# Kernel tuning notes

Measured on AMD Instinct MI355X. Metric: run time of the kernel, lower is better.

The kernel has to match this reference:

```python
import jax, jax.numpy as jnp
import numpy as np

D = 128  # time-encoder dimension == attention embed_dim


def harmonic_encode(ts, basis_freq):
    # ts: (N,) -> (N, D); phases are zero in the original module
    m = ts[:, None] * basis_freq[None, :]
    return jnp.sqrt(1.0 / D) * jnp.concatenate([jnp.cos(m), jnp.sin(m)], axis=1)


def mha_1head(q, k, mask, Wq, bq, Wk, bk, Wv, bv, Wo, bo):
    # Single-head nn.MultiheadAttention. q: (T, D) queries (torch batch dim),
    # k: (S, D) shared keys/values (original repeats these T times; same math),
    # mask: (T, S) True = masked out (key_padding_mask semantics).
    qp = q @ Wq.T + bq
    kp = k @ Wk.T + bk
    vp = k @ Wv.T + bv
    scores = jnp.einsum('td,sd->ts', qp, kp) / jnp.sqrt(jnp.asarray(D, q.dtype))
    scores = jnp.where(mask, -jnp.inf, scores)
    attn = jax.nn.softmax(scores, axis=-1)  # (T, S)
    return (attn @ vp) @ Wo.T + bo


def setup_inputs() -> dict:
    key = jax.random.key(0)
    ks = jax.random.split(key, 24)
    T, L, V = 4096, 8192, 1000
    s = 1.0 / np.sqrt(D)
    inp = {
        't': jax.random.uniform(ks[0], (T,), jnp.float32),
        'e_nodes_ts': jax.random.uniform(ks[1], (L,), jnp.float32),
        'e_nodes_exp': jax.random.randint(ks[2], (L,), 0, V),
        'e_node_target': jax.random.randint(ks[3], (1,), 0, V),
        'basis_freq': jnp.asarray(1.0 / 5.0 ** np.linspace(1, 9, D // 2), jnp.float32),
        'phi': jnp.ones((1,), jnp.float32),
        'W_lin': jax.random.normal(ks[4], (1, 2 * D), jnp.float32) * 0.05,
        'b_lin': jnp.zeros((1,), jnp.float32),
    }
    kidx = 5
    for suf in ('_s', '_n'):
        for nm in ('Wq', 'Wk', 'Wv', 'Wo'):
            inp[nm + suf] = jax.random.normal(ks[kidx], (D, D), jnp.float32) * s
            kidx += 1
        for nm in ('bq', 'bk', 'bv', 'bo'):
            inp[nm + suf] = jnp.zeros((D,), jnp.float32)
    return inp


def reference(t, e_nodes_ts, e_nodes_exp, e_node_target, basis_freq, phi, W_lin, b_lin,
              Wq_s, Wk_s, Wv_s, Wo_s, bq_s, bk_s, bv_s, bo_s,
              Wq_n, Wk_n, Wv_n, Wo_n, bq_n, bk_n, bv_n, bo_n):
    # prepend sentinels exactly as the torch forward does
    ts_all = jnp.concatenate([jnp.zeros((2,), e_nodes_ts.dtype), e_nodes_ts])      # (S,)
    exp_all = jnp.concatenate([jnp.full((1,), -1, e_nodes_exp.dtype), e_node_target, e_nodes_exp])  # (S,)

    phi_t = harmonic_encode(t, basis_freq)        # (T, D)
    phi_ts = harmonic_encode(ts_all, basis_freq)  # (S, D)

    pad = ts_all[None, :] > t[:, None]            # (T, S) future events masked
    self_mask = pad | (exp_all != e_node_target[0])[None, :]
    neig_mask = pad | (exp_all == e_node_target[0])[None, :]

    out_s = mha_1head(phi_t, phi_ts, self_mask, Wq_s, bq_s, Wk_s, bk_s, Wv_s, bv_s, Wo_s, bo_s)
    out_n = mha_1head(phi_t, phi_ts, neig_mask, Wq_n, bq_n, Wk_n, bk_n, Wv_n, bv_n, Wo_n, bo_n)
    atten_output = jnp.concatenate([out_s, out_n], axis=1)  # (T, 2D)

    lam = atten_output @ W_lin.T + b_lin          # (T, 1)
    x = lam * phi
    x = jnp.where(x > 20.0, 20.0, x)              # clamp as in soft_plus()
    lambdav = (1.0 / phi) * jnp.log1p(jnp.exp(x))
    return lambdav, atten_output
```

## Files before the change

### kernel.cpp

```cpp
#include <hip/hip_runtime.h>

#define T_Q 4096
#define S_TOT 8194
#define S_ALLOC 8256
#define SELF_CAP 128
#define NSEG 11
#define NSLOT 12
#define NCH64 129
#define SCALE 0.08838834764831843f
#define NEG_BIG -1.0e30f
#define TS_INF 3.0e38f

typedef __attribute__((ext_vector_type(8))) short short8;
typedef __attribute__((ext_vector_type(4))) float f32x4;
typedef __attribute__((ext_vector_type(4))) unsigned short ush4;
typedef unsigned short ush;
typedef unsigned int uint32;
typedef unsigned long long u64;

static __device__ __forceinline__ ush f2bf(float f) {
    unsigned int u = __float_as_uint(f);
    u += 0x7FFFu + ((u >> 16) & 1u);
    return (ush)(u >> 16);
}

__global__ __launch_bounds__(256) void prep_kernel(
    const float* __restrict__ t, const float* __restrict__ ets,
    const int* __restrict__ exps, const int* __restrict__ tgtp,
    const float* __restrict__ bf,
    const float* __restrict__ Wo_s, const float* __restrict__ Wv_s, const float* __restrict__ bv_s,
    const float* __restrict__ Wo_n, const float* __restrict__ Wv_n, const float* __restrict__ bv_n,
    const float* __restrict__ Wq_s, const float* __restrict__ Wq_n,
    const float* __restrict__ Wk_s, const float* __restrict__ Wk_n,
    ush* __restrict__ phi_t, ush* __restrict__ phi_ts,
    float* __restrict__ ts_pad, float* __restrict__ ts1, int* __restrict__ perm1,
    u64* __restrict__ maskbits, ush* __restrict__ Wb, float* __restrict__ bvo)
{
    __shared__ float red[256];
    __shared__ int swcnt[4];
    __shared__ int stot;
    int bid = blockIdx.x, tid = threadIdx.x;

    if (bid < 3088) {
        int R = bid * 4 + (tid >> 6);
        int j = tid & 63;
        float x; ush* dst;
        if (R < T_Q) { x = t[R]; dst = phi_t + (size_t)R * 128; }
        else {
            int s = R - T_Q;
            x = (s < 2) ? 0.0f : ((s < S_TOT) ? ets[s - 2] : 0.0f);
            dst = phi_ts + (size_t)s * 128;
        }
        float m = x * bf[j];
        dst[j]      = f2bf(cosf(m) * SCALE);
        dst[64 + j] = f2bf(sinf(m) * SCALE);
    } else if (bid == 3088) {
        int tgt = tgtp[0];
        for (int i = tid; i < S_ALLOC; i += 256)
            ts_pad[i] = (i < 2) ? 0.f : ((i < S_TOT) ? ets[i - 2] : TS_INF);
        int w4 = tid >> 6, lane = tid & 63;
        int cbeg = w4 * 33, cend = (w4 == 3) ? NCH64 : (cbeg + 33);
        u64 ltm = ((u64)1 << lane) - 1ull;
        int cnt = 0;
        for (int ch = cbeg; ch < cend; ++ch) {
            int s = ch * 64 + lane;
            bool m = (s < S_TOT) && ((s == 1) || (s >= 2 && exps[s - 2] == tgt));
            u64 b = __ballot(m);
            if (lane == 0) maskbits[ch] = b;
            cnt += __popcll(b);
        }
        if (lane == 0) swcnt[w4] = cnt;
        __syncthreads();
        if (tid == 0) {
            int a = 0;
            #pragma unroll
            for (int i = 0; i < 4; ++i) { int tc = swcnt[i]; swcnt[i] = a; a += tc; }
            stot = a;
        }
        __syncthreads();
        int off2 = swcnt[w4];
        for (int ch = cbeg; ch < cend; ++ch) {
            int s = ch * 64 + lane;
            bool m = (s < S_TOT) && ((s == 1) || (s >= 2 && exps[s - 2] == tgt));
            u64 b = __ballot(m);
            if (m) {
                int p = off2 + __popcll(b & ltm);
                if (p < SELF_CAP) { perm1[p] = s; ts1[p] = (s >= 2) ? ets[s - 2] : 0.f; }
            }
            off2 += __popcll(b);
        }
        __syncthreads();
        int st = stot > SELF_CAP ? SELF_CAP : stot;
        for (int i = st + tid; i < SELF_CAP; i += 256) { perm1[i] = 0; ts1[i] = TS_INF; }
    } else if (bid < 3217) {
        int row = bid - 3089;
        int h = tid >> 7, col = tid & 127;
        const float* Wo = h ? Wo_n : Wo_s;
        const float* Wv = h ? Wv_n : Wv_s;
        const float* bv = h ? bv_n : bv_s;
        float acc = 0.f;
        for (int jj = 0; jj < 128; ++jj) acc += Wo[row * 128 + jj] * Wv[jj * 128 + col];
        Wb[(size_t)(4 + h) * 16384 + row * 128 + col] = f2bf(acc);
        red[tid] = Wo[row * 128 + col] * bv[col];
        __syncthreads();
        for (int off = 64; off > 0; off >>= 1) {
            if ((tid & 127) < off) red[tid] += red[tid + off];
            __syncthreads();
        }
        if ((tid & 127) == 0) bvo[h * 128 + row] = red[tid];
    } else {
        int idx = (bid - 3217) * 256 + tid;
        int which = idx >> 14, e = idx & 16383;
        const float* src;
        switch (which) {
            case 0: src = Wq_s; break; case 1: src = Wq_n; break;
            case 2: src = Wk_s; break; default: src = Wk_n; break;
        }
        Wb[idx] = f2bf(src[e]);
    }
}

__global__ __launch_bounds__(256) void proj_kernel(
    const ush* __restrict__ phi_t, const ush* __restrict__ phi_ts, const ush* __restrict__ Wb,
    const float* __restrict__ bq_s, const float* __restrict__ bq_n,
    const float* __restrict__ bk_s, const float* __restrict__ bk_n,
    const float* __restrict__ bvo, const int* __restrict__ perm1,
    ush* __restrict__ qp, ush* __restrict__ kpc, ush* __restrict__ vpoT)
{
    int y = blockIdx.y;
    const float* b; int M; const int* perm = nullptr; int ldv = 0;
    const ush* in = phi_ts;
    ush* out = nullptr; ush* outT = nullptr;
    switch (y) {
        case 0: b = bq_s;      M = T_Q; in = phi_t; out = qp; break;
        case 1: b = bq_n;      M = T_Q; in = phi_t; out = qp + (size_t)T_Q * 128; break;
        case 2: b = bk_s;      M = SELF_CAP; perm = perm1; out = kpc; break;
        case 3: b = bk_n;      M = S_ALLOC;  out = kpc + (size_t)SELF_CAP * 128; break;
        case 4: b = bvo;       M = SELF_CAP; perm = perm1; outT = vpoT; ldv = SELF_CAP; break;
        default:b = bvo + 128; M = S_ALLOC;  outT = vpoT + (size_t)SELF_CAP * 128; ldv = S_ALLOC; break;
    }
    int mbase = blockIdx.x * 64 + (int)(threadIdx.x >> 6) * 16;
    if (mbase >= M) return;
    int lane = threadIdx.x & 63, u = lane >> 4, c = lane & 15;
    const ush* arow = perm ? (in + (size_t)perm[mbase + c] * 128)
                           : (in + (size_t)(mbase + c) * 128);
    short8 af[4];
    #pragma unroll
    for (int ks = 0; ks < 4; ++ks) af[ks] = *(const short8*)(arow + ks * 32 + u * 8);
    const ush* W = Wb + (size_t)y * 16384;
    #pragma unroll
    for (int nt = 0; nt < 8; ++nt) {
        int ncol = nt * 16 + c;
        float bval = b[ncol];
        f32x4 acc = {bval, bval, bval, bval};
        #pragma unroll
        for (int ks = 0; ks < 4; ++ks) {
            short8 bf8 = *(const short8*)(W + ncol * 128 + ks * 32 + u * 8);
            acc = __builtin_amdgcn_mfma_f32_16x16x32_bf16(af[ks], bf8, acc, 0, 0, 0);
        }
        if (outT) {
            ush4 pk;
            #pragma unroll
            for (int r = 0; r < 4; ++r) pk[r] = f2bf(acc[r]);
            *(ush4*)(outT + (size_t)ncol * ldv + mbase + u * 4) = pk;
        } else {
            #pragma unroll
            for (int r = 0; r < 4; ++r)
                out[(size_t)(mbase + u * 4 + r) * 128 + ncol] = f2bf(acc[r]);
        }
    }
}

__global__ __launch_bounds__(256, 2) void attn_kernel(
    const ush* __restrict__ qp, const ush* __restrict__ kpc, const ush* __restrict__ vpoT,
    const float* __restrict__ ts_pad, const float* __restrict__ ts1,
    const u64* __restrict__ maskbits, const float* __restrict__ tq,
    float* __restrict__ Opart, float* __restrict__ mpart, float* __restrict__ lpart)
{
    int bid = blockIdx.x;
    int head, qb, slot, t0, t1;
    if (bid < 32 * NSEG) {
        head = 1; int seg = bid >> 5; qb = bid & 31; slot = seg;
        t0 = seg * NCH64 / NSEG; t1 = (seg + 1) * NCH64 / NSEG;
    } else {
        head = 0; qb = bid - 32 * NSEG; slot = NSEG; t0 = 0; t1 = SELF_CAP / 64;
    }
    const ush* kph = kpc  + (head ? (size_t)SELF_CAP * 128 : 0);
    const ush* vph = vpoT + (head ? (size_t)SELF_CAP * 128 : 0);
    const int ld = head ? S_ALLOC : SELF_CAP;
    const float* tsh = head ? ts_pad : ts1;
    const ush* qph = qp + (head ? (size_t)T_Q * 128 : 0);

    __shared__ __align__(16) ush K2[2][64 * 128];
    __shared__ __align__(16) ush V1[128 * 64];
    __shared__ float tsb[2][64];

    int tid = threadIdx.x, w = tid >> 6, lane = tid & 63;
    int u = lane >> 4, c = lane & 15;
    int qrow0 = qb * 128 + w * 32;
    int sbase = (lane & 48) + ((lane & 48) >> 2);

    short8 qf[2][4];
    #pragma unroll
    for (int qg = 0; qg < 2; ++qg) {
        const ush* qr = qph + (size_t)(qrow0 + qg * 16 + c) * 128;
        #pragma unroll
        for (int ks = 0; ks < 4; ++ks) qf[qg][ks] = *(const short8*)(qr + ks * 32 + u * 8);
    }
    float t_c[2] = { tq[qrow0 + c], tq[qrow0 + 16 + c] };

    f32x4 Ov[2][8];
    #pragma unroll
    for (int qg = 0; qg < 2; ++qg)
        #pragma unroll
        for (int dt = 0; dt < 8; ++dt) Ov[qg][dt] = (f32x4){0.f, 0.f, 0.f, 0.f};
    float mrow[2] = {NEG_BIG, NEG_BIG}, lrow[2] = {0.f, 0.f};

    short8 kreg[4], vreg[4]; float tsreg = 0.f;
    int kr = tid >> 2, kq = tid & 3;
    int vd = tid >> 1, vh = tid & 1;

    auto LOADT = [&](int t) {
        int kb = t * 64;
        const ush* src = kph + (size_t)(kb + kr) * 128 + kq * 32;
        #pragma unroll
        for (int i = 0; i < 4; ++i) kreg[i] = *(const short8*)(src + i * 8);
        const ush* vsrc = vph + (size_t)vd * ld + kb + vh * 32;
        #pragma unroll
        for (int i = 0; i < 4; ++i) vreg[i] = *(const short8*)(vsrc + i * 8);
        if (tid < 64) tsreg = tsh[kb + tid];
    };
    auto WRITE_K = [&](int b) {
        #pragma unroll
        for (int i = 0; i < 4; ++i)
            *(short8*)&K2[b][kr * 128 + (((kq * 4 + i) ^ (kr & 7)) << 3)] = kreg[i];
        if (tid < 64) tsb[b][tid] = tsreg;
    };
    auto WRITE_V = [&]() {
        #pragma unroll
        for (int i = 0; i < 4; ++i)
            *(short8*)&V1[vd * 64 + (((vh * 4 + i) ^ (vd & 7)) << 3)] = vreg[i];
    };

    LOADT(t0); WRITE_K(0); WRITE_V();
    __syncthreads();

    for (int t = t0; t < t1; ++t) {
        int cur = (t - t0) & 1;
        bool pre = (t + 1 < t1);
        u64 mk = head ? maskbits[t] : 0ull;
        if (pre) LOADT(t + 1);

        float sc[2][4][4];
        #pragma unroll
        for (int ct = 0; ct < 4; ++ct) {
            short8 kf[4];
            int row = ct * 16 + c;
            #pragma unroll
            for (int ks = 0; ks < 4; ++ks)
                kf[ks] = *(const short8*)&K2[cur][row * 128 + (((ks * 4 + u) ^ (row & 7)) << 3)];
            f32x4 acc0 = {0.f, 0.f, 0.f, 0.f}, acc1 = {0.f, 0.f, 0.f, 0.f};
            #pragma unroll
            for (int ks = 0; ks < 4; ++ks) {
                acc0 = __builtin_amdgcn_mfma_f32_16x16x32_bf16(kf[ks], qf[0][ks], acc0, 0, 0, 0);
                acc1 = __builtin_amdgcn_mfma_f32_16x16x32_bf16(kf[ks], qf[1][ks], acc1, 0, 0, 0);
            }
            f32x4 ts4 = *(const f32x4*)&tsb[cur][ct * 16 + u * 4];
            uint32 mh = (uint32)(mk >> (ct * 16 + u * 4));
            #pragma unroll
            for (int r = 0; r < 4; ++r) {
                bool em = (mh >> r) & 1u;
                sc[0][ct][r] = (em || ts4[r] > t_c[0]) ? NEG_BIG : acc0[r] * SCALE;
                sc[1][ct][r] = (em || ts4[r] > t_c[1]) ? NEG_BIG : acc1[r] * SCALE;
            }
        }
        if (pre) WRITE_K(cur ^ 1);

        short8 pfq[2][2];
        #pragma unroll
        for (int qg = 0; qg < 2; ++qg) {
            float mt = sc[qg][0][0];
            #pragma unroll
            for (int ct = 0; ct < 4; ++ct)
                #pragma unroll
                for (int r = 0; r < 4; ++r) mt = fmaxf(mt, sc[qg][ct][r]);
            mt = fmaxf(mt, __shfl_xor(mt, 16));
            mt = fmaxf(mt, __shfl_xor(mt, 32));
            if (__any(mt > mrow[qg])) {
                float mnew = fmaxf(mrow[qg], mt);
                float sf = __expf(mrow[qg] - mnew);
                mrow[qg] = mnew;
                lrow[qg] *= sf;
                float sfr[4];
                #pragma unroll
                for (int r = 0; r < 4; ++r) sfr[r] = __shfl(sf, sbase + r);
                #pragma unroll
                for (int dt = 0; dt < 8; ++dt) {
                    Ov[qg][dt][0] *= sfr[0]; Ov[qg][dt][1] *= sfr[1];
                    Ov[qg][dt][2] *= sfr[2]; Ov[qg][dt][3] *= sfr[3];
                }
            }
            float p[4][4], s16 = 0.f;
            #pragma unroll
            for (int ct = 0; ct < 4; ++ct)
                #pragma unroll
                for (int r = 0; r < 4; ++r) { p[ct][r] = __expf(sc[qg][ct][r] - mrow[qg]); s16 += p[ct][r]; }
            s16 += __shfl_xor(s16, 16);
            s16 += __shfl_xor(s16, 32);
            lrow[qg] += s16;

            uint32 q0[4], q1[4];
            #pragma unroll
            for (int ct = 0; ct < 4; ++ct) {
                asm("v_cvt_pk_bf16_f32 %0, %1, %2" : "=v"(q0[ct]) : "v"(p[ct][0]), "v"(p[ct][1]));
                asm("v_cvt_pk_bf16_f32 %0, %1, %2" : "=v"(q1[ct]) : "v"(p[ct][2]), "v"(p[ct][3]));
            }
            #pragma unroll
            for (int ksl = 0; ksl < 2; ++ksl) {
                uint32 a0 = q0[2 * ksl], b0 = q0[2 * ksl + 1];
                uint32 a1 = q1[2 * ksl], b1 = q1[2 * ksl + 1];
                asm("v_permlane32_swap_b32 %0, %1" : "+v"(a0), "+v"(b0));
                asm("v_permlane16_swap_b32 %0, %1" : "+v"(a0), "+v"(b0));
                asm("v_permlane32_swap_b32 %0, %1" : "+v"(a1), "+v"(b1));
                asm("v_permlane16_swap_b32 %0, %1" : "+v"(a1), "+v"(b1));
                union { uint32 w4[4]; short8 s8; } pk_;
                pk_.w4[0] = a0; pk_.w4[1] = a1; pk_.w4[2] = b0; pk_.w4[3] = b1;
                pfq[qg][ksl] = pk_.s8;
            }
        }

        #pragma unroll
        for (int ksl = 0; ksl < 2; ++ksl)
            #pragma unroll
            for (int dt = 0; dt < 8; ++dt) {
                int d = dt * 16 + c;
                short8 vf = *(const short8*)&V1[d * 64 + (((ksl * 4 + u) ^ (d & 7)) << 3)];
                Ov[0][dt] = __builtin_amdgcn_mfma_f32_16x16x32_bf16(pfq[0][ksl], vf, Ov[0][dt], 0, 0, 0);
                Ov[1][dt] = __builtin_amdgcn_mfma_f32_16x16x32_bf16(pfq[1][ksl], vf, Ov[1][dt], 0, 0, 0);
            }

        __syncthreads();
        if (pre) WRITE_V();
        __syncthreads();
    }

    size_t rbase = (size_t)slot * T_Q + qrow0;
    #pragma unroll
    for (int qg = 0; qg < 2; ++qg)
        #pragma unroll
        for (int dt = 0; dt < 8; ++dt)
            #pragma unroll
            for (int r = 0; r < 4; ++r)
                Opart[(rbase + qg * 16 + u * 4 + r) * 128 + dt * 16 + c] = Ov[qg][dt][r];
    if (u == 0) {
        mpart[rbase + c] = mrow[0];      lpart[rbase + c] = lrow[0];
        mpart[rbase + 16 + c] = mrow[1]; lpart[rbase + 16 + c] = lrow[1];
    }
}

__global__ __launch_bounds__(256) void combine_kernel(
    const float* __restrict__ Opart, const float* __restrict__ mpart, const float* __restrict__ lpart,
    const float* __restrict__ bo_s, const float* __restrict__ bo_n,
    const float* __restrict__ Wl, const float* __restrict__ bl,
    const float* __restrict__ phi, float* __restrict__ outp)
{
    int row = blockIdx.x, tid = threadIdx.x;
    float outv;
    if (tid < 128) {
        size_t rb = (size_t)NSEG * T_Q + row;
        outv = Opart[rb * 128 + tid] / lpart[rb] + bo_s[tid];
    } else {
        int d = tid - 128;
        float M = NEG_BIG;
        #pragma unroll
        for (int z = 0; z < NSEG; ++z) M = fmaxf(M, mpart[(size_t)z * T_Q + row]);
        float L = 0.f, O = 0.f;
        #pragma unroll
        for (int z = 0; z < NSEG; ++z) {
            size_t rb = (size_t)z * T_Q + row;
            float wz = __expf(mpart[rb] - M);
            L += wz * lpart[rb];
            O += wz * Opart[rb * 128 + d];
        }
        outv = O / L + bo_n[d];
    }
    outp[T_Q + (size_t)row * 256 + tid] = outv;

    float dot = outv * Wl[tid];
    #pragma unroll
    for (int off = 1; off < 64; off <<= 1) dot += __shfl_xor(dot, off);
    __shared__ float wsum[4];
    if ((tid & 63) == 0) wsum[tid >> 6] = dot;
    __syncthreads();
    if (tid == 0) {
        float s = wsum[0] + wsum[1] + wsum[2] + wsum[3];
        float ph = phi[0];
        float x = (s + bl[0]) * ph;
        x = fminf(x, 20.0f);
        outp[row] = log1pf(__expf(x)) / ph;
    }
}

extern "C" void kernel_launch(void* const* d_in, const int* in_sizes, int n_in,
                              void* d_out, int out_size, void* d_ws, size_t ws_size,
                              hipStream_t stream) {
    (void)in_sizes; (void)n_in; (void)out_size; (void)ws_size;
    const float* t    = (const float*)d_in[0];
    const float* ets  = (const float*)d_in[1];
    const int*   exps = (const int*)d_in[2];
    const int*   tgt  = (const int*)d_in[3];
    const float* bfq  = (const float*)d_in[4];
    const float* phi  = (const float*)d_in[5];
    const float* Wlin = (const float*)d_in[6];
    const float* blin = (const float*)d_in[7];
    const float* Wq_s = (const float*)d_in[8];
    const float* Wk_s = (const float*)d_in[9];
    const float* Wv_s = (const float*)d_in[10];
    const float* Wo_s = (const float*)d_in[11];
    const float* bq_s = (const float*)d_in[12];
    const float* bk_s = (const float*)d_in[13];
    const float* bv_s = (const float*)d_in[14];
    const float* bo_s = (const float*)d_in[15];
    const float* Wq_n = (const float*)d_in[16];
    const float* Wk_n = (const float*)d_in[17];
    const float* Wv_n = (const float*)d_in[18];
    const float* Wo_n = (const float*)d_in[19];
    const float* bq_n = (const float*)d_in[20];
    const float* bk_n = (const float*)d_in[21];
    const float* bv_n = (const float*)d_in[22];
    const float* bo_n = (const float*)d_in[23];

    char* ws = (char*)d_ws;
    size_t off = 0;
    auto alloc = [&](size_t bytes) { void* p = ws + off; off += (bytes + 255) & ~(size_t)255; return p; };
    ush* phi_t  = (ush*)alloc((size_t)T_Q * 128 * 2);
    ush* phi_ts = (ush*)alloc((size_t)S_ALLOC * 128 * 2);
    ush* qpb    = (ush*)alloc((size_t)2 * T_Q * 128 * 2);
    ush* kpc    = (ush*)alloc((size_t)(SELF_CAP + S_ALLOC) * 128 * 2);
    ush* vpoT   = (ush*)alloc((size_t)128 * (SELF_CAP + S_ALLOC) * 2);
    int*    perm1 = (int*)   alloc((size_t)SELF_CAP * 4);
    float*  ts1   = (float*) alloc((size_t)SELF_CAP * 4);
    float*  ts_pad= (float*) alloc((size_t)S_ALLOC * 4);
    u64*    maskb = (u64*)   alloc((size_t)NCH64 * 8);
    float*  bvo   = (float*) alloc((size_t)2 * 128 * 4);
    ush*    Wb    = (ush*)   alloc((size_t)6 * 16384 * 2);
    float*  Opart = (float*) alloc((size_t)NSLOT * T_Q * 128 * 4);
    float*  mpart = (float*) alloc((size_t)NSLOT * T_Q * 4);
    float*  lpart = (float*) alloc((size_t)NSLOT * T_Q * 4);

    float* outp = (float*)d_out;

    prep_kernel<<<dim3(3473), dim3(256), 0, stream>>>(
        t, ets, exps, tgt, bfq, Wo_s, Wv_s, bv_s, Wo_n, Wv_n, bv_n,
        Wq_s, Wq_n, Wk_s, Wk_n, phi_t, phi_ts, ts_pad, ts1, perm1, maskb, Wb, bvo);
    proj_kernel<<<dim3(129, 6), dim3(256), 0, stream>>>(
        phi_t, phi_ts, Wb, bq_s, bq_n, bk_s, bk_n, bvo, perm1, qpb, kpc, vpoT);
    attn_kernel<<<dim3(32 * NSEG + 32), dim3(256), 0, stream>>>(
        qpb, kpc, vpoT, ts_pad, ts1, maskb, t, Opart, mpart, lpart);
    combine_kernel<<<dim3(T_Q), dim3(256), 0, stream>>>(
        Opart, mpart, lpart, bo_s, bo_n, Wlin, blin, phi, outp);
}
```

Baseline: 106.6 us.

## Split neighbor attention into more segments, raise occupancy, store bf16 partials

Doubles the number of key segments for the neighbor head and remaps block indices with an interleaved order. Drops K double-buffering so the attention kernel uses less LDS and can run 3 blocks per SM. It now writes partial outputs in bf16, halving partial traffic in the combine step. Prep stages the expert ids in LDS as 16-bit values and unrolls the Wo·Wv product loop. The trade-offs are lost load/compute overlap on K, more partials to merge, and bf16 rounding of the unnormalized partial sums.

Result: slower. 170.2 us (+59.7%).

```diff
diff --git a/kernel.cpp b/kernel.cpp
--- a/kernel.cpp
+++ b/kernel.cpp
@@ -4,8 +4,8 @@
 #define S_TOT 8194
 #define S_ALLOC 8256
 #define SELF_CAP 128
-#define NSEG 11
-#define NSLOT 12
+#define NSEG 23
+#define NSLOT 24
 #define NCH64 129
 #define SCALE 0.08838834764831843f
 #define NEG_BIG -1.0e30f
@@ -22,6 +22,9 @@
     unsigned int u = __float_as_uint(f);
     u += 0x7FFFu + ((u >> 16) & 1u);
     return (ush)(u >> 16);
+}
+static __device__ __forceinline__ float bf2f(ush u) {
+    return __uint_as_float(((unsigned int)u) << 16);
 }
 
 __global__ __launch_bounds__(256) void prep_kernel(
@@ -36,9 +39,10 @@
     float* __restrict__ ts_pad, float* __restrict__ ts1, int* __restrict__ perm1,
     u64* __restrict__ maskbits, ush* __restrict__ Wb, float* __restrict__ bvo)
 {
-    __shared__ float red[256];
+    __shared__ __align__(16) ush es[8192];
     __shared__ int swcnt[4];
     __shared__ int stot;
+    float* red = (float*)es;
     int bid = blockIdx.x, tid = threadIdx.x;
 
     if (bid < 3088) {
@@ -56,15 +60,21 @@
         dst[64 + j] = f2bf(sinf(m) * SCALE);
     } else if (bid == 3088) {
         int tgt = tgtp[0];
+        for (int i = tid * 4; i < S_TOT - 2; i += 1024) {
+            int4 v = *(const int4*)(exps + i);
+            es[i] = (ush)v.x; es[i + 1] = (ush)v.y; es[i + 2] = (ush)v.z; es[i + 3] = (ush)v.w;
+        }
         for (int i = tid; i < S_ALLOC; i += 256)
             ts_pad[i] = (i < 2) ? 0.f : ((i < S_TOT) ? ets[i - 2] : TS_INF);
+        __syncthreads();
+        ush tgt16 = (ush)tgt;
         int w4 = tid >> 6, lane = tid & 63;
         int cbeg = w4 * 33, cend = (w4 == 3) ? NCH64 : (cbeg + 33);
         u64 ltm = ((u64)1 << lane) - 1ull;
         int cnt = 0;
         for (int ch = cbeg; ch < cend; ++ch) {
             int s = ch * 64 + lane;
-            bool m = (s < S_TOT) && ((s == 1) || (s >= 2 && exps[s - 2] == tgt));
+            bool m = (s < S_TOT) && ((s == 1) || (s >= 2 && es[s - 2] == tgt16));
             u64 b = __ballot(m);
             if (lane == 0) maskbits[ch] = b;
             cnt += __popcll(b);
@@ -81,7 +91,7 @@
         int off2 = swcnt[w4];
         for (int ch = cbeg; ch < cend; ++ch) {
             int s = ch * 64 + lane;
-            bool m = (s < S_TOT) && ((s == 1) || (s >= 2 && exps[s - 2] == tgt));
+            bool m = (s < S_TOT) && ((s == 1) || (s >= 2 && es[s - 2] == tgt16));
             u64 b = __ballot(m);
             if (m) {
                 int p = off2 + __popcll(b & ltm);
@@ -99,6 +109,7 @@
         const float* Wv = h ? Wv_n : Wv_s;
         const float* bv = h ? bv_n : bv_s;
         float acc = 0.f;
+        #pragma unroll 8
         for (int jj = 0; jj < 128; ++jj) acc += Wo[row * 128 + jj] * Wv[jj * 128 + col];
         Wb[(size_t)(4 + h) * 16384 + row * 128 + col] = f2bf(acc);
         red[tid] = Wo[row * 128 + col] * bv[col];
@@ -171,13 +182,13 @@
     }
 }
 
-__global__ __launch_bounds__(256, 2) void attn_kernel(
+__global__ __launch_bounds__(256, 3) void attn_kernel(
     const ush* __restrict__ qp, const ush* __restrict__ kpc, const ush* __restrict__ vpoT,
     const float* __restrict__ ts_pad, const float* __restrict__ ts1,
     const u64* __restrict__ maskbits, const float* __restrict__ tq,
-    float* __restrict__ Opart, float* __restrict__ mpart, float* __restrict__ lpart)
+    ush* __restrict__ Opart, float* __restrict__ mpart, float* __restrict__ lpart)
 {
-    int bid = blockIdx.x;
+    int bid = ((int)blockIdx.x & 7) * 96 + ((int)blockIdx.x >> 3);
     int head, qb, slot, t0, t1;
     if (bid < 32 * NSEG) {
         head = 1; int seg = bid >> 5; qb = bid & 31; slot = seg;
@@ -191,9 +202,9 @@
     const float* tsh = head ? ts_pad : ts1;
     const ush* qph = qp + (head ? (size_t)T_Q * 128 : 0);
 
-    __shared__ __align__(16) ush K2[2][64 * 128];
+    __shared__ __align__(16) ush K1[64 * 128];
     __shared__ __align__(16) ush V1[128 * 64];
-    __shared__ float tsb[2][64];
+    __shared__ float tsb[64];
 
     int tid = threadIdx.x, w = tid >> 6, lane = tid & 63;
     int u = lane >> 4, c = lane & 15;
@@ -230,23 +241,20 @@
         for (int i = 0; i < 4; ++i) vreg[i] = *(const short8*)(vsrc + i * 8);
         if (tid < 64) tsreg = tsh[kb + tid];
     };
-    auto WRITE_K = [&](int b) {
+    auto WRITE_KV = [&]() {
         #pragma unroll
         for (int i = 0; i < 4; ++i)
-            *(short8*)&K2[b][kr * 128 + (((kq * 4 + i) ^ (kr & 7)) << 3)] = kreg[i];
-        if (tid < 64) tsb[b][tid] = tsreg;
-    };
-    auto WRITE_V = [&]() {
+            *(short8*)&K1[kr * 128 + (((kq * 4 + i) ^ (kr & 7)) << 3)] = kreg[i];
         #pragma unroll
         for (int i = 0; i < 4; ++i)
             *(short8*)&V1[vd * 64 + (((vh * 4 + i) ^ (vd & 7)) << 3)] = vreg[i];
+        if (tid < 64) tsb[tid] = tsreg;
     };
 
-    LOADT(t0); WRITE_K(0); WRITE_V();
+    LOADT(t0); WRITE_KV();
     __syncthreads();
 
     for (int t = t0; t < t1; ++t) {
-        int cur = (t - t0) & 1;
         bool pre = (t + 1 < t1);
         u64 mk = head ? maskbits[t] : 0ull;
         if (pre) LOADT(t + 1);
@@ -258,14 +266,14 @@
             int row = ct * 16 + c;
             #pragma unroll
             for (int ks = 0; ks < 4; ++ks)
-                kf[ks] = *(const short8*)&K2[cur][row * 128 + (((ks * 4 + u) ^ (row & 7)) << 3)];
+                kf[ks] = *(const short8*)&K1[row * 128 + (((ks * 4 + u) ^ (row & 7)) << 3)];
             f32x4 acc0 = {0.f, 0.f, 0.f, 0.f}, acc1 = {0.f, 0.f, 0.f, 0.f};
             #pragma unroll
             for (int ks = 0; ks < 4; ++ks) {
                 acc0 = __builtin_amdgcn_mfma_f32_16x16x32_bf16(kf[ks], qf[0][ks], acc0, 0, 0, 0);
                 acc1 = __builtin_amdgcn_mfma_f32_16x16x32_bf16(kf[ks], qf[1][ks], acc1, 0, 0, 0);
             }
-            f32x4 ts4 = *(const f32x4*)&tsb[cur][ct * 16 + u * 4];
+            f32x4 ts4 = *(const f32x4*)&tsb[ct * 16 + u * 4];
             uint32 mh = (uint32)(mk >> (ct * 16 + u * 4));
             #pragma unroll
             for (int r = 0; r < 4; ++r) {
@@ -274,7 +282,6 @@
                 sc[1][ct][r] = (em || ts4[r] > t_c[1]) ? NEG_BIG : acc1[r] * SCALE;
             }
         }
-        if (pre) WRITE_K(cur ^ 1);
 
         short8 pfq[2][2];
         #pragma unroll
@@ -340,7 +347,7 @@
             }
 
         __syncthreads();
-        if (pre) WRITE_V();
+        if (pre) WRITE_KV();
         __syncthreads();
     }
 
@@ -351,7 +358,7 @@
         for (int dt = 0; dt < 8; ++dt)
             #pragma unroll
             for (int r = 0; r < 4; ++r)
-                Opart[(rbase + qg * 16 + u * 4 + r) * 128 + dt * 16 + c] = Ov[qg][dt][r];
+                Opart[(rbase + qg * 16 + u * 4 + r) * 128 + dt * 16 + c] = f2bf(Ov[qg][dt][r]);
     if (u == 0) {
         mpart[rbase + c] = mrow[0];      lpart[rbase + c] = lrow[0];
         mpart[rbase + 16 + c] = mrow[1]; lpart[rbase + 16 + c] = lrow[1];
@@ -359,7 +366,7 @@
 }
 
 __global__ __launch_bounds__(256) void combine_kernel(
-    const float* __restrict__ Opart, const float* __restrict__ mpart, const float* __restrict__ lpart,
+    const ush* __restrict__ Opart, const float* __restrict__ mpart, const float* __restrict__ lpart,
     const float* __restrict__ bo_s, const float* __restrict__ bo_n,
     const float* __restrict__ Wl, const float* __restrict__ bl,
     const float* __restrict__ phi, float* __restrict__ outp)
@@ -368,7 +375,7 @@
     float outv;
     if (tid < 128) {
         size_t rb = (size_t)NSEG * T_Q + row;
-        outv = Opart[rb * 128 + tid] / lpart[rb] + bo_s[tid];
+        outv = bf2f(Opart[rb * 128 + tid]) / lpart[rb] + bo_s[tid];
     } else {
         int d = tid - 128;
         float M = NEG_BIG;
@@ -380,7 +387,7 @@
             size_t rb = (size_t)z * T_Q + row;
             float wz = __expf(mpart[rb] - M);
             L += wz * lpart[rb];
-            O += wz * Opart[rb * 128 + d];
+            O += wz * bf2f(Opart[rb * 128 + d]);
         }
         outv = O / L + bo_n[d];
     }
@@ -444,7 +451,7 @@
     u64*    maskb = (u64*)   alloc((size_t)NCH64 * 8);
     float*  bvo   = (float*) alloc((size_t)2 * 128 * 4);
     ush*    Wb    = (ush*)   alloc((size_t)6 * 16384 * 2);
-    float*  Opart = (float*) alloc((size_t)NSLOT * T_Q * 128 * 4);
+    ush*    Opart = (ush*)   alloc((size_t)NSLOT * T_Q * 128 * 2);
     float*  mpart = (float*) alloc((size_t)NSLOT * T_Q * 4);
     float*  lpart = (float*) alloc((size_t)NSLOT * T_Q * 4);
 
```
